# Kernel tuning notes

Measured on AMD Instinct MI355X. Metric: run time of the kernel, lower is better.

The kernel has to match this reference:

```python
import jax, jax.numpy as jnp
import numpy as np

B = 128            # number of subgraphs (one head, one tail each)
NODES_PER_G = 64
N = B * NODES_PER_G  # 8192 total nodes
E = 131072           # total edges in the batched graph
NUM_RELS = 200
D = 64               # rel_emb_dim
EMB = 64             # emb_dim
L = 3                # num_gcn_layers (jumping-knowledge concat)
REPR = L * EMB       # 192, g.ndata['repr'] feature width
LINK_MODE = 6


def setup_inputs() -> dict:
    key = jax.random.key(0)
    ks = jax.random.split(key, 10)
    node_repr = jax.random.normal(ks[0], (N, REPR), jnp.float32)
    edge_src = jax.random.randint(ks[1], (E,), 0, N, dtype=jnp.int32)
    edge_dst = jax.random.randint(ks[2], (E,), 0, N, dtype=jnp.int32)
    edge_type = jax.random.randint(ks[3], (E,), 0, NUM_RELS, dtype=jnp.int32)
    rel_labels = jax.random.randint(ks[4], (B,), 0, NUM_RELS, dtype=jnp.int32)
    node_graph_id = (jnp.arange(N) // NODES_PER_G).astype(jnp.int32)
    head_ids = (jnp.arange(B) * NODES_PER_G).astype(jnp.int32)   # node with id==1 per graph
    tail_ids = head_ids + 1                                      # node with id==2 per graph
    rel_emb_w = jax.random.normal(ks[5], (NUM_RELS, D), jnp.float32)
    W_reld = jax.random.normal(ks[6], (LINK_MODE, D, D), jnp.float32) * 0.05
    b_reld = jnp.zeros((LINK_MODE, D), jnp.float32)
    Wc = jax.random.normal(ks[7], (D, 2 * D), jnp.float32) * 0.05
    bc = jnp.zeros((D,), jnp.float32)
    Wf = jax.random.normal(ks[8], (1, 3 * REPR + D), jnp.float32) * 0.05
    bf = jnp.zeros((1,), jnp.float32)
    return {
        'node_repr': node_repr, 'rel_emb_w': rel_emb_w, 'W_reld': W_reld,
        'b_reld': b_reld, 'Wc': Wc, 'bc': bc, 'Wf': Wf, 'bf': bf,
        'edge_src': edge_src, 'edge_dst': edge_dst, 'edge_type': edge_type,
        'rel_labels': rel_labels, 'node_graph_id': node_graph_id,
        'head_ids': head_ids, 'tail_ids': tail_ids,
    }


def reference(node_repr, rel_emb_w, W_reld, b_reld, Wc, bc, Wf, bf,
              edge_src, edge_dst, edge_type, rel_labels, node_graph_id,
              head_ids, tail_ids):
    f32 = jnp.float32
    nb = head_ids.shape[0]
    # Six edge connection modes, [B, E] each (row b selects edges incident to
    # the head/tail node of subgraph b).
    io = (edge_dst[None, :] == head_ids[:, None]).astype(f32)  # in_edge_out
    oo = (edge_src[None, :] == head_ids[:, None]).astype(f32)  # out_edge_out
    ii = (edge_dst[None, :] == tail_ids[:, None]).astype(f32)  # in_edge_in
    oi = (edge_src[None, :] == tail_ids[:, None]).astype(f32)  # out_edge_in
    m5 = oo * ii   # edge_mode_5: head -> tail edges
    m6 = io * oi   # edge_mode_6: tail -> head edges
    modes = jnp.stack([io - m6, oo - m5, ii - m5, oi - m6, m5, m6])  # [6,B,E]
    norms = modes.sum(-1, keepdims=True) + 1e-30                      # [6,B,1]
    # Per-mode linear transform of relation embeddings, then aggregate.
    rel_feat = rel_emb_w[edge_type]                                   # [E,D]
    trans = jnp.einsum('ed,mfd->mef', rel_feat, W_reld) + b_reld[:, None, :]  # [6,E,D]
    contrib = jnp.einsum('mbe,med->mbd', modes, trans) / norms        # [6,B,D]
    rel_neighbor = contrib.mean(0)                                    # sum(...)/link_mode
    rel_final = jnp.concatenate([rel_neighbor, rel_emb_w[rel_labels]], -1) @ Wc.T + bc
    rel_final = jax.nn.relu(rel_final)
    rel_final = rel_final / jnp.maximum(
        jnp.linalg.norm(rel_final, axis=-1, keepdims=True), 1e-12)
    # mean_nodes(g, 'repr') per subgraph
    g_sum = jax.ops.segment_sum(node_repr, node_graph_id, num_segments=nb)
    counts = jax.ops.segment_sum(jnp.ones((node_repr.shape[0],), f32),
                                 node_graph_id, num_segments=nb)
    g_out = g_sum / counts[:, None]
    g_rep = jnp.concatenate(
        [g_out, node_repr[head_ids], node_repr[tail_ids], rel_final], -1)
    return g_rep @ Wf.T + bf   # [B, 1]
```

## Files before the change

kernel.cpp:

```cpp
#include <hip/hip_runtime.h>

#define NGRAPH 128
#define NEDGE  131072
#define DIM    64
#define REPRW  192

__global__ __launch_bounds__(256) void zero_ws_kernel(float* __restrict__ ws, int n) {
    int i = blockIdx.x * 256 + threadIdx.x;
    if (i < n) ws[i] = 0.0f;
}

__global__ __launch_bounds__(256) void edge_scatter_kernel(
    const int* __restrict__ esrc, const int* __restrict__ edst,
    const int* __restrict__ etype, const float* __restrict__ rel_emb,
    float* __restrict__ S, float* __restrict__ cnt)
{
    int e = blockIdx.x * 256 + threadIdx.x;
    int lane = threadIdx.x & 63;
    int s = esrc[e];
    int d = edst[e];
    int et = etype[e];

    int dl = d & 63, sl = s & 63;
    int b_d = d >> 6, b_s = s >> 6;

    int mode_d = -1;
    if (dl == 0)      mode_d = (s == d + 1) ? 5 : 0;
    else if (dl == 1) mode_d = (s == d - 1) ? -1 : 2;

    int mode_s = -1;
    if (sl == 0)      mode_s = (d == s + 1) ? 4 : 1;
    else if (sl == 1) mode_s = (d == s - 1) ? -1 : 3;

    unsigned long long mask = __ballot(mode_d >= 0);
    while (mask) {
        int l = __builtin_ctzll(mask); mask &= mask - 1;
        int mm = __shfl(mode_d, l);
        int bb = __shfl(b_d, l);
        int tt = __shfl(et, l);
        atomicAdd(&S[(mm * NGRAPH + bb) * DIM + lane], rel_emb[tt * DIM + lane]);
        if (lane == 0) atomicAdd(&cnt[mm * NGRAPH + bb], 1.0f);
    }
    mask = __ballot(mode_s >= 0);
    while (mask) {
        int l = __builtin_ctzll(mask); mask &= mask - 1;
        int mm = __shfl(mode_s, l);
        int bb = __shfl(b_s, l);
        int tt = __shfl(et, l);
        atomicAdd(&S[(mm * NGRAPH + bb) * DIM + lane], rel_emb[tt * DIM + lane]);
        if (lane == 0) atomicAdd(&cnt[mm * NGRAPH + bb], 1.0f);
    }
}

__global__ __launch_bounds__(256) void finalize_kernel(
    const float* __restrict__ node_repr, const float* __restrict__ rel_emb,
    const float* __restrict__ W_reld, const float* __restrict__ b_reld,
    const float* __restrict__ Wc, const float* __restrict__ bc,
    const float* __restrict__ Wf, const float* __restrict__ bf,
    const int* __restrict__ rel_labels, const int* __restrict__ head_ids,
    const int* __restrict__ tail_ids,
    const float* __restrict__ S, const float* __restrict__ cnt,
    float* __restrict__ out)
{
    int b = blockIdx.x;
    int tid = threadIdx.x;

    __shared__ float sh_grep[640];
    __shared__ __align__(16) float sh_S[6 * 64];
    __shared__ float sh_cnt[6];
    __shared__ float sh_rn[64];
    __shared__ float sh_red[256];

    for (int i = tid; i < 6 * 64; i += 256)
        sh_S[i] = S[((i >> 6) * NGRAPH + b) * DIM + (i & 63)];
    if (tid < 6) sh_cnt[tid] = cnt[tid * NGRAPH + b];

    int h = head_ids[b], t = tail_ids[b];
    if (tid < REPRW) {
        const float* base = node_repr + (size_t)b * 64 * REPRW + tid;
        float acc = 0.0f;
        #pragma unroll 8
        for (int n = 0; n < 64; n++) acc += base[(size_t)n * REPRW];
        sh_grep[tid]           = acc * (1.0f / 64.0f);
        sh_grep[192 + tid]     = node_repr[(size_t)h * REPRW + tid];
        sh_grep[384 + tid]     = node_repr[(size_t)t * REPRW + tid];
    }
    __syncthreads();

    if (tid < 64) {
        float acc = 0.0f;
        #pragma unroll
        for (int m = 0; m < 6; m++) {
            float c = sh_cnt[m];
            float inv = 1.0f / (c + 1e-30f);
            const float4* Wrow = (const float4*)(W_reld + (m * 64 + tid) * 64);
            const float4* Sv   = (const float4*)(sh_S + m * 64);
            float dotv = 0.0f;
            #pragma unroll
            for (int k = 0; k < 16; k++) {
                float4 w = Wrow[k];
                float4 sv = Sv[k];
                dotv += w.x * sv.x + w.y * sv.y + w.z * sv.z + w.w * sv.w;
            }
            acc += (dotv + c * b_reld[m * 64 + tid]) * inv;
        }
        sh_rn[tid] = acc * (1.0f / 6.0f);
    }
    __syncthreads();

    if (tid < 64) {
        const float* rl = rel_emb + rel_labels[b] * DIM;
        const float* Wrow = Wc + tid * 128;
        float z = bc[tid];
        #pragma unroll 8
        for (int j = 0; j < 64; j++) z += sh_rn[j] * Wrow[j];
        #pragma unroll 8
        for (int j = 0; j < 64; j++) z += rl[j] * Wrow[64 + j];
        z = fmaxf(z, 0.0f);
        float sq = z * z;
        #pragma unroll
        for (int off = 32; off >= 1; off >>= 1) sq += __shfl_xor(sq, off);
        float nrm = fmaxf(sqrtf(sq), 1e-12f);
        sh_grep[576 + tid] = z / nrm;
    }
    __syncthreads();

    float p = 0.0f;
    for (int i = tid; i < 640; i += 256) p += sh_grep[i] * Wf[i];
    sh_red[tid] = p;
    __syncthreads();
    for (int s2 = 128; s2 > 0; s2 >>= 1) {
        if (tid < s2) sh_red[tid] += sh_red[tid + s2];
        __syncthreads();
    }
    if (tid == 0) out[b] = sh_red[0] + bf[0];
}

extern "C" void kernel_launch(void* const* d_in, const int* in_sizes, int n_in,
                              void* d_out, int out_size, void* d_ws, size_t ws_size,
                              hipStream_t stream) {
    (void)in_sizes; (void)n_in; (void)out_size; (void)ws_size;

    const float* node_repr = (const float*)d_in[0];
    const float* rel_emb   = (const float*)d_in[1];
    const float* W_reld    = (const float*)d_in[2];
    const float* b_reld    = (const float*)d_in[3];
    const float* Wc        = (const float*)d_in[4];
    const float* bc        = (const float*)d_in[5];
    const float* Wf        = (const float*)d_in[6];
    const float* bf        = (const float*)d_in[7];
    const int*   esrc      = (const int*)d_in[8];
    const int*   edst      = (const int*)d_in[9];
    const int*   etype     = (const int*)d_in[10];
    const int*   rel_labels= (const int*)d_in[11];
    const int*   head_ids  = (const int*)d_in[13];
    const int*   tail_ids  = (const int*)d_in[14];

    float* S   = (float*)d_ws;
    float* cnt = S + 6 * NGRAPH * DIM;
    int nz = 6 * NGRAPH * DIM + 6 * NGRAPH;

    zero_ws_kernel<<<(nz + 255) / 256, 256, 0, stream>>>(S, nz);
    edge_scatter_kernel<<<NEDGE / 256, 256, 0, stream>>>(esrc, edst, etype, rel_emb, S, cnt);
    finalize_kernel<<<NGRAPH, 256, 0, stream>>>(node_repr, rel_emb, W_reld, b_reld,
                                                Wc, bc, Wf, bf, rel_labels, head_ids,
                                                tail_ids, S, cnt, (float*)d_out);
}
```

Baseline: 116.2 us.

## Fuse edge scatter and finalize into one per-graph kernel with shared-memory aggregation

Replaces the zero, global-atomic edge scatter and finalize kernels with a single kernel of 1024 threads per subgraph. Each block scans the whole edge list, collects the edges that touch its head or tail into a shared-memory list, and aggregates relation embeddings with shared atomics. It also parallelises the node-mean, per-mode transform and final reduction across more threads, and stages Wc in padded shared memory. This removes two launches and the contended global atomics, but every block now re-reads the full edge arrays.

New measurement: 112.3 us. 1.03x faster.

```diff
diff --git a/kernel.cpp b/kernel.cpp
--- a/kernel.cpp
+++ b/kernel.cpp
@@ -4,113 +4,143 @@
 #define NEDGE  131072
 #define DIM    64
 #define REPRW  192
+#define NTHREADS 1024
+#define MAXHITS 1024
 
-__global__ __launch_bounds__(256) void zero_ws_kernel(float* __restrict__ ws, int n) {
-    int i = blockIdx.x * 256 + threadIdx.x;
-    if (i < n) ws[i] = 0.0f;
-}
-
-__global__ __launch_bounds__(256) void edge_scatter_kernel(
-    const int* __restrict__ esrc, const int* __restrict__ edst,
-    const int* __restrict__ etype, const float* __restrict__ rel_emb,
-    float* __restrict__ S, float* __restrict__ cnt)
-{
-    int e = blockIdx.x * 256 + threadIdx.x;
-    int lane = threadIdx.x & 63;
-    int s = esrc[e];
-    int d = edst[e];
-    int et = etype[e];
-
-    int dl = d & 63, sl = s & 63;
-    int b_d = d >> 6, b_s = s >> 6;
-
-    int mode_d = -1;
-    if (dl == 0)      mode_d = (s == d + 1) ? 5 : 0;
-    else if (dl == 1) mode_d = (s == d - 1) ? -1 : 2;
-
-    int mode_s = -1;
-    if (sl == 0)      mode_s = (d == s + 1) ? 4 : 1;
-    else if (sl == 1) mode_s = (d == s - 1) ? -1 : 3;
-
-    unsigned long long mask = __ballot(mode_d >= 0);
-    while (mask) {
-        int l = __builtin_ctzll(mask); mask &= mask - 1;
-        int mm = __shfl(mode_d, l);
-        int bb = __shfl(b_d, l);
-        int tt = __shfl(et, l);
-        atomicAdd(&S[(mm * NGRAPH + bb) * DIM + lane], rel_emb[tt * DIM + lane]);
-        if (lane == 0) atomicAdd(&cnt[mm * NGRAPH + bb], 1.0f);
-    }
-    mask = __ballot(mode_s >= 0);
-    while (mask) {
-        int l = __builtin_ctzll(mask); mask &= mask - 1;
-        int mm = __shfl(mode_s, l);
-        int bb = __shfl(b_s, l);
-        int tt = __shfl(et, l);
-        atomicAdd(&S[(mm * NGRAPH + bb) * DIM + lane], rel_emb[tt * DIM + lane]);
-        if (lane == 0) atomicAdd(&cnt[mm * NGRAPH + bb], 1.0f);
-    }
-}
-
-__global__ __launch_bounds__(256) void finalize_kernel(
+__global__ __launch_bounds__(NTHREADS) void fused_graph_kernel(
     const float* __restrict__ node_repr, const float* __restrict__ rel_emb,
     const float* __restrict__ W_reld, const float* __restrict__ b_reld,
     const float* __restrict__ Wc, const float* __restrict__ bc,
     const float* __restrict__ Wf, const float* __restrict__ bf,
-    const int* __restrict__ rel_labels, const int* __restrict__ head_ids,
-    const int* __restrict__ tail_ids,
-    const float* __restrict__ S, const float* __restrict__ cnt,
+    const int* __restrict__ esrc, const int* __restrict__ edst,
+    const int* __restrict__ etype, const int* __restrict__ rel_labels,
+    const int* __restrict__ head_ids, const int* __restrict__ tail_ids,
     float* __restrict__ out)
 {
-    int b = blockIdx.x;
-    int tid = threadIdx.x;
+    const int b    = blockIdx.x;
+    const int tid  = threadIdx.x;
+    const int base = b << 6;
+    const int wave = tid >> 6;
+    const int lane = tid & 63;
 
+    __shared__ __align__(16) float shS[6 * 64];
+    __shared__ float shCnt[6];
+    __shared__ int   shList[MAXHITS];
+    __shared__ int   shNHits;
     __shared__ float sh_grep[640];
-    __shared__ __align__(16) float sh_S[6 * 64];
-    __shared__ float sh_cnt[6];
+    __shared__ float sh_part[4 * 192];
+    __shared__ float sh_v[6 * 64];
     __shared__ float sh_rn[64];
-    __shared__ float sh_red[256];
+    __shared__ float sh_Wc[64 * 129];
+    __shared__ float sh_red[16];
 
-    for (int i = tid; i < 6 * 64; i += 256)
-        sh_S[i] = S[((i >> 6) * NGRAPH + b) * DIM + (i & 63)];
-    if (tid < 6) sh_cnt[tid] = cnt[tid * NGRAPH + b];
+    if (tid < 384) shS[tid] = 0.0f;
+    if (tid < 6)   shCnt[tid] = 0.0f;
+    if (tid == 0)  shNHits = 0;
+    __syncthreads();
 
-    int h = head_ids[b], t = tail_ids[b];
-    if (tid < REPRW) {
-        const float* base = node_repr + (size_t)b * 64 * REPRW + tid;
-        float acc = 0.0f;
-        #pragma unroll 8
-        for (int n = 0; n < 64; n++) acc += base[(size_t)n * REPRW];
-        sh_grep[tid]           = acc * (1.0f / 64.0f);
-        sh_grep[192 + tid]     = node_repr[(size_t)h * REPRW + tid];
-        sh_grep[384 + tid]     = node_repr[(size_t)t * REPRW + tid];
+    {
+        int r = tid / 192, col = tid - r * 192;
+        if (tid < 768) {
+            const float* p = node_repr + (size_t)(base + r * 16) * REPRW + col;
+            float a = 0.0f;
+            #pragma unroll
+            for (int n = 0; n < 16; n++) a += p[(size_t)n * REPRW];
+            sh_part[r * 192 + col] = a;
+        }
+        if (tid < 192) {
+            sh_grep[192 + tid] = node_repr[(size_t)head_ids[b] * REPRW + tid];
+            sh_grep[384 + tid] = node_repr[(size_t)tail_ids[b] * REPRW + tid];
+        }
+    }
+
+    {
+        const int4* s4 = (const int4*)esrc;
+        const int4* d4 = (const int4*)edst;
+        for (int i = tid; i < NEDGE / 4; i += NTHREADS) {
+            int4 ss = s4[i];
+            int4 dd = d4[i];
+            #pragma unroll
+            for (int c = 0; c < 4; c++) {
+                int s = (c == 0) ? ss.x : (c == 1) ? ss.y : (c == 2) ? ss.z : ss.w;
+                int d = (c == 0) ? dd.x : (c == 1) ? dd.y : (c == 2) ? dd.z : dd.w;
+                bool hd = (unsigned)(d - base) < 2u;
+                bool hs = (unsigned)(s - base) < 2u;
+                if (hd | hs) {
+                    int et = etype[4 * i + c];
+                    if (hd) {
+                        if (d == base) {
+                            int m = (s == base + 1) ? 5 : 0;
+                            int idx = atomicAdd(&shNHits, 1);
+                            if (idx < MAXHITS) shList[idx] = (m << 16) | et;
+                            atomicAdd(&shCnt[m], 1.0f);
+                        } else if (s != base) {
+                            int idx = atomicAdd(&shNHits, 1);
+                            if (idx < MAXHITS) shList[idx] = (2 << 16) | et;
+                            atomicAdd(&shCnt[2], 1.0f);
+                        }
+                    }
+                    if (hs) {
+                        if (s == base) {
+                            int m = (d == base + 1) ? 4 : 1;
+                            int idx = atomicAdd(&shNHits, 1);
+                            if (idx < MAXHITS) shList[idx] = (m << 16) | et;
+                            atomicAdd(&shCnt[m], 1.0f);
+                        } else if (d != base) {
+                            int idx = atomicAdd(&shNHits, 1);
+                            if (idx < MAXHITS) shList[idx] = (3 << 16) | et;
+                            atomicAdd(&shCnt[3], 1.0f);
+                        }
+                    }
+                }
+            }
+        }
+    }
+    __syncthreads();
+
+    {
+        int nh = shNHits < MAXHITS ? shNHits : MAXHITS;
+        for (int h = wave; h < nh; h += 16) {
+            int ent = shList[h];
+            int m = ent >> 16, t = ent & 0xffff;
+            atomicAdd(&shS[m * 64 + lane], rel_emb[t * 64 + lane]);
+        }
+        if (tid < 192)
+            sh_grep[tid] = (sh_part[tid] + sh_part[192 + tid] +
+                            sh_part[384 + tid] + sh_part[576 + tid]) * (1.0f / 64.0f);
+    }
+    __syncthreads();
+
+    if (tid < 384) {
+        int m = wave, f = lane;
+        const float4* Wrow = (const float4*)(W_reld + (m * 64 + f) * 64);
+        const float4* Sv   = (const float4*)(shS + m * 64);
+        float dot = 0.0f;
+        #pragma unroll
+        for (int k = 0; k < 16; k++) {
+            float4 w = Wrow[k];
+            float4 sv = Sv[k];
+            dot += w.x * sv.x + w.y * sv.y + w.z * sv.z + w.w * sv.w;
+        }
+        float cm = shCnt[m];
+        sh_v[m * 64 + f] = (dot + cm * b_reld[m * 64 + f]) / (cm + 1e-30f);
+    } else {
+        for (int j = tid - 384; j < 64 * 128; j += NTHREADS - 384) {
+            int row = j >> 7, col = j & 127;
+            sh_Wc[row * 129 + col] = Wc[j];
+        }
     }
     __syncthreads();
 
     if (tid < 64) {
-        float acc = 0.0f;
-        #pragma unroll
-        for (int m = 0; m < 6; m++) {
-            float c = sh_cnt[m];
-            float inv = 1.0f / (c + 1e-30f);
-            const float4* Wrow = (const float4*)(W_reld + (m * 64 + tid) * 64);
-            const float4* Sv   = (const float4*)(sh_S + m * 64);
-            float dotv = 0.0f;
-            #pragma unroll
-            for (int k = 0; k < 16; k++) {
-                float4 w = Wrow[k];
-                float4 sv = Sv[k];
-                dotv += w.x * sv.x + w.y * sv.y + w.z * sv.z + w.w * sv.w;
-            }
-            acc += (dotv + c * b_reld[m * 64 + tid]) * inv;
-        }
-        sh_rn[tid] = acc * (1.0f / 6.0f);
+        sh_rn[tid] = (sh_v[tid] + sh_v[64 + tid] + sh_v[128 + tid] +
+                      sh_v[192 + tid] + sh_v[256 + tid] + sh_v[320 + tid]) * (1.0f / 6.0f);
     }
     __syncthreads();
 
     if (tid < 64) {
         const float* rl = rel_emb + rel_labels[b] * DIM;
-        const float* Wrow = Wc + tid * 128;
+        const float* Wrow = sh_Wc + tid * 129;
         float z = bc[tid];
         #pragma unroll 8
         for (int j = 0; j < 64; j++) z += sh_rn[j] * Wrow[j];
@@ -125,21 +155,25 @@
     }
     __syncthreads();
 
-    float p = 0.0f;
-    for (int i = tid; i < 640; i += 256) p += sh_grep[i] * Wf[i];
-    sh_red[tid] = p;
+    if (tid < 640) {
+        float p = sh_grep[tid] * Wf[tid];
+        #pragma unroll
+        for (int off = 32; off >= 1; off >>= 1) p += __shfl_xor(p, off);
+        if (lane == 0) sh_red[wave] = p;
+    }
     __syncthreads();
-    for (int s2 = 128; s2 > 0; s2 >>= 1) {
-        if (tid < s2) sh_red[tid] += sh_red[tid + s2];
-        __syncthreads();
+    if (tid == 0) {
+        float acc = bf[0];
+        #pragma unroll
+        for (int w = 0; w < 10; w++) acc += sh_red[w];
+        out[b] = acc;
     }
-    if (tid == 0) out[b] = sh_red[0] + bf[0];
 }
 
 extern "C" void kernel_launch(void* const* d_in, const int* in_sizes, int n_in,
                               void* d_out, int out_size, void* d_ws, size_t ws_size,
                               hipStream_t stream) {
-    (void)in_sizes; (void)n_in; (void)out_size; (void)ws_size;
+    (void)in_sizes; (void)n_in; (void)out_size; (void)d_ws; (void)ws_size;
 
     const float* node_repr = (const float*)d_in[0];
     const float* rel_emb   = (const float*)d_in[1];
@@ -156,13 +190,7 @@
     const int*   head_ids  = (const int*)d_in[13];
     const int*   tail_ids  = (const int*)d_in[14];
 
-    float* S   = (float*)d_ws;
-    float* cnt = S + 6 * NGRAPH * DIM;
-    int nz = 6 * NGRAPH * DIM + 6 * NGRAPH;
-
-    zero_ws_kernel<<<(nz + 255) / 256, 256, 0, stream>>>(S, nz);
-    edge_scatter_kernel<<<NEDGE / 256, 256, 0, stream>>>(esrc, edst, etype, rel_emb, S, cnt);
-    finalize_kernel<<<NGRAPH, 256, 0, stream>>>(node_repr, rel_emb, W_reld, b_reld,
-                                                Wc, bc, Wf, bf, rel_labels, head_ids,
-                                                tail_ids, S, cnt, (float*)d_out);
+    fused_graph_kernel<<<NGRAPH, NTHREADS, 0, stream>>>(
+        node_repr, rel_emb, W_reld, b_reld, Wc, bc, Wf, bf,
+        esrc, edst, etype, rel_labels, head_ids, tail_ids, (float*)d_out);
 }
```
